# Optimization experiments

Hardware: AMD Instinct MI355X
Metric: run time of the kernel (lower is better)

## Reference

```python
import math
import jax, jax.numpy as jnp
import numpy as np

B, NH, L0 = 16, 128, 16384
KS, STRIDE = 4, 2
INIT_GATE_BIAS = 1.0


def _num_steps(L, ks, stride):
    # number of reduce steps until any N <= L reaches N <= 1 (matches torch N recurrence)
    d, n = 0, L
    while True:
        n = (max(n - ks, 0) + stride - 1) // stride + 1
        d += 1
        if n <= 1:
            return d


def setup_inputs() -> dict:
    key = jax.random.key(0)
    k1, k2, k3, k4 = jax.random.split(key, 4)
    h = jax.random.normal(k1, (B, NH, L0), dtype=jnp.float32)
    N = jax.random.randint(k2, (B,), 1, L0 + 1, dtype=jnp.int32)
    cin = NH + 1  # depth_variant adds one channel
    bound = 1.0 / math.sqrt(cin * KS)
    W = jax.random.uniform(k3, (3 * NH, cin, KS), minval=-bound, maxval=bound, dtype=jnp.float32)
    b = jax.random.uniform(k4, (3 * NH,), minval=-bound, maxval=bound, dtype=jnp.float32)
    b = b.at[2 * NH:].set(INIT_GATE_BIAS)
    return {"h": h, "N": N, "W": W, "b": b}


def _step(h, N, depth, W, b):
    Bb, _, Lc = h.shape
    # depth channel (depth_variant=True), then mask invalid positions (mask applied after concat, as in torch)
    d = jnp.full((Bb, 1, Lc), math.log1p(depth), dtype=h.dtype)
    hh = jnp.concatenate([h, d], axis=1)
    mask = (jnp.arange(Lc) < N[:, None]).astype(hh.dtype)  # [B, Lc]
    hh = hh * mask[:, None, :]
    # right-pad so conv covers all valid positions
    if Lc < KS:
        pad_r = KS - Lc
    elif (Lc - KS) % STRIDE != 0:
        pad_r = STRIDE - (Lc - KS) % STRIDE
    else:
        pad_r = 0
    if pad_r:
        hh = jnp.pad(hh, ((0, 0), (0, 0), (0, pad_r)))
    lrg = jax.lax.conv_general_dilated(
        hh, W, window_strides=(STRIDE,), padding='VALID',
        dimension_numbers=('NCH', 'OIH', 'NCH')) + b[None, :, None]
    l = lrg[:, :NH]
    r = jnp.tanh(lrg[:, NH:2 * NH])
    g = jax.nn.sigmoid(lrg[:, 2 * NH:])
    h_new = l * g + r * (1.0 - g)
    m = jnp.maximum(N - KS, 0)
    N_new = (m + STRIDE - 1) // STRIDE + 1  # ceil(clamp(N-ks,0)/stride)+1
    return h_new, N_new


def reference(h, N, W, b):
    # Fixed-depth unroll: instead of compacting the batch (dynamic shapes), run
    # every sample for all D steps and record its row at the step it finishes.
    # Torch output order = samples sorted stably by finish depth (boolean-index
    # compaction preserves original relative order), reproduced via stable argsort.
    D = _num_steps(h.shape[2], KS, STRIDE)
    Bb = h.shape[0]
    out_h = jnp.zeros((Bb, NH), dtype=h.dtype)
    finish = jnp.full((Bb,), D, dtype=jnp.int32)
    done = jnp.zeros((Bb,), dtype=bool)
    for depth in range(D):
        h, N = _step(h, N, depth, W, b)
        newly = (~done) & (N <= 1)
        out_h = jnp.where(newly[:, None], h[:, :, 0], out_h)
        finish = jnp.where(newly, depth, finish)
        done = done | newly
    order = jnp.argsort(finish)  # stable by default in jax
    return out_h[order]
```

## Files before the change

kernel.cpp:

```cpp
#include <hip/hip_runtime.h>
#include <math.h>

typedef _Float16 f16_t;
typedef _Float16 f16x8 __attribute__((ext_vector_type(8)));
typedef _Float16 f16x4 __attribute__((ext_vector_type(4)));
typedef float    f32x4 __attribute__((ext_vector_type(4)));

#define NHC 128
#define NBATCH 16
#define JT 64
#define THREADS 512
#define TTHREADS 256
#define L0LEN 16384
#define LDSROWPITCH 272
#define LDSREGION (66*LDSROWPITCH)
#define TREG (130*LDSROWPITCH)

__device__ __host__ __forceinline__ int nstep_f(int n){ int m = n - 4; m = m < 0 ? 0 : m; return ((m + 1) >> 1) + 1; }

__global__ void prep_kernel(const float* __restrict__ W, const float* __restrict__ bin,
                            f16_t* __restrict__ Wt, float* __restrict__ Pp, float* __restrict__ biasf)
{
    int c = blockIdx.x;
    int i = threadIdx.x;
    #pragma unroll
    for (int k = 0; k < 4; k++)
        Wt[((size_t)k*384 + c)*128 + i] = (f16_t)W[((size_t)c*129 + i)*4 + k];
    if (i == 0) {
        float s = 0.f;
        Pp[c*5 + 0] = 0.f;
        #pragma unroll
        for (int k = 0; k < 4; k++) { s += W[((size_t)c*129 + 128)*4 + k]; Pp[c*5 + k + 1] = s; }
        biasf[c] = bin[c];
    }
}

template<int CTM>
__device__ __forceinline__ void gemm_tap(f32x4 (&acc)[3][4], const f16_t* __restrict__ Wt,
                                         const char* ldsIn, int arow, int n16, int q)
{
    #pragma unroll 1
    for (int k = 0; k < 4; k++) {
        const f16_t* ab = Wt + ((size_t)k*384 + arow)*128 + q*8;
        f16x8 a0[4], a1[4], a2[4];
        #pragma unroll
        for (int kc = 0; kc < 4; kc++) {
            a0[kc] = *(const f16x8*)(ab + kc*32);
            a1[kc] = *(const f16x8*)(ab + 16384 + kc*32);
            a2[kc] = *(const f16x8*)(ab + 32768 + kc*32);
        }
        const char* bb0 = ldsIn + (k&1)*LDSREGION + ((k>>1) + n16)*LDSROWPITCH + q*16;
        #pragma unroll
        for (int kc = 0; kc < 4; kc++) {
            #pragma unroll
            for (int ct = 0; ct < CTM; ct++) {
                f16x8 bb = *(const f16x8*)(bb0 + ct*(16*LDSROWPITCH) + kc*64);
                acc[0][ct] = __builtin_amdgcn_mfma_f32_16x16x32_f16(a0[kc], bb, acc[0][ct], 0, 0, 0);
                acc[1][ct] = __builtin_amdgcn_mfma_f32_16x16x32_f16(a1[kc], bb, acc[1][ct], 0, 0, 0);
                acc[2][ct] = __builtin_amdgcn_mfma_f32_16x16x32_f16(a2[kc], bb, acc[2][ct], 0, 0, 0);
            }
        }
    }
}

__device__ __forceinline__ void load_biasp(float (&biasr)[3][4], float (&pfull)[3][4],
                                           const float* __restrict__ biasf,
                                           const float* __restrict__ Pp, int cw)
{
    #pragma unroll
    for (int s = 0; s < 3; s++)
        #pragma unroll
        for (int r = 0; r < 4; r++) {
            int row = s*128 + cw + r;
            biasr[s][r] = biasf[row];
            pfull[s][r] = Pp[row*5 + 4];
        }
}

__global__ __launch_bounds__(THREADS) void conv_kernel(
    const float* __restrict__ h, const f16_t* __restrict__ Xin, f16_t* __restrict__ Xout,
    const f16_t* __restrict__ Wt, const float* __restrict__ Pp,
    const float* __restrict__ biasf, const int* __restrict__ N0,
    float* __restrict__ outbuf,
    int t, int inCols, int outCols, float dval)
{
    __shared__ alignas(16) char ldsX[2*LDSREGION];
    const int b  = blockIdx.y;
    const int j0 = blockIdx.x * JT;
    const int tid = threadIdx.x;
    int Nt = N0[b];
    for (int s = 0; s < t; s++) Nt = nstep_f(Nt);
    const int Nt1 = nstep_f(Nt);

    f16_t* XoutB = Xout + ((size_t)b*outCols + j0)*NHC;
    if (j0 >= Nt1) {
        if (j0 <= Nt1 + 1 && tid < 32) {
            float4 z = {0.f,0.f,0.f,0.f};
            ((float4*)XoutB)[tid] = z;
        }
        return;
    }

    if (t == 0) {
        const float* hB = h + (size_t)b*NHC*L0LEN;
        const int P0 = 2*j0;
        const int jpr = tid & 63;
        const int s8  = tid >> 6;
        #pragma unroll
        for (int cg = 0; cg < 16; cg++) {
            int c = cg*8 + s8;
            int p = P0 + jpr*2;
            float2 v = {0.f, 0.f};
            if (p + 1 < Nt)      v = *(const float2*)(hB + (size_t)c*L0LEN + p);
            else if (p < Nt)     v.x = hB[(size_t)c*L0LEN + p];
            char* wb = ldsX + jpr*LDSROWPITCH + c*2;
            *(f16_t*)(wb)             = (f16_t)v.x;
            *(f16_t*)(wb + LDSREGION) = (f16_t)v.y;
        }
        if (tid < 128) {
            int c = tid;
            int p = P0 + 128;
            float2 v = {0.f, 0.f};
            if (p + 1 < Nt)      v = *(const float2*)(hB + (size_t)c*L0LEN + p);
            else if (p < Nt)     v.x = hB[(size_t)c*L0LEN + p];
            char* wb = ldsX + 64*LDSROWPITCH + c*2;
            *(f16_t*)(wb)             = (f16_t)v.x;
            *(f16_t*)(wb + LDSREGION) = (f16_t)v.y;
        }
    } else {
        const char* XinB = (const char*)(Xin + ((size_t)b*inCols + 2*(size_t)j0)*NHC);
        const int maxrow = inCols - 2*j0;
        for (int it = 0; it < 5; ++it) {
            int idx = it*THREADS + tid;
            if (idx < 130*16) {
                int row = idx >> 4, cb = (idx & 15) * 16;
                float4 v = {0.f,0.f,0.f,0.f};
                if (row < maxrow) v = *(const float4*)(XinB + row*256 + cb);
                *(float4*)(ldsX + (row&1)*LDSREGION + (row>>1)*LDSROWPITCH + cb) = v;
            }
        }
    }
    __syncthreads();

    const int w    = tid >> 6;
    const int lane = tid & 63;
    const int n16  = lane & 15;
    const int q    = lane >> 4;
    const int arow = w*16 + n16;
    const int cw   = w*16 + q*4;

    f32x4 acc[3][4] = {};
    int ctm = (Nt1 - j0 + 15) >> 4; if (ctm > 4) ctm = 4;
    switch (ctm) {
    case 1:  gemm_tap<1>(acc, Wt, ldsX, arow, n16, q); break;
    case 2:  gemm_tap<2>(acc, Wt, ldsX, arow, n16, q); break;
    case 3:  gemm_tap<3>(acc, Wt, ldsX, arow, n16, q); break;
    default: gemm_tap<4>(acc, Wt, ldsX, arow, n16, q); break;
    }

    float biasr[3][4], pfull[3][4];
    load_biasp(biasr, pfull, biasf, Pp, cw);

    bool newly = (Nt1 == 1) && (t == 0 || Nt > 1);
    bool record = newly && (j0 == 0);
    float* outrow = outbuf + b*NHC;

    #pragma unroll
    for (int ct = 0; ct < 4; ct++) {
        int j = j0 + ct*16 + n16;
        int cnt = Nt - 2*j; cnt = cnt < 0 ? 0 : (cnt > 4 ? 4 : cnt);
        bool zero = (j >= Nt1);
        float hv[4];
        #pragma unroll
        for (int r = 0; r < 4; r++) {
            float d0, d1, d2;
            if (cnt == 4)      { d0 = pfull[0][r]; d1 = pfull[1][r]; d2 = pfull[2][r]; }
            else if (cnt == 0) { d0 = 0.f; d1 = 0.f; d2 = 0.f; }
            else { int rw = cw + r; d0 = Pp[rw*5 + cnt]; d1 = Pp[(128+rw)*5 + cnt]; d2 = Pp[(256+rw)*5 + cnt]; }
            float lv = acc[0][ct][r] + biasr[0][r] + dval*d0;
            float rp = acc[1][ct][r] + biasr[1][r] + dval*d1;
            float gp = acc[2][ct][r] + biasr[2][r] + dval*d2;
            float e2 = __expf(2.f*rp);
            float rv = 1.f - 2.f/(e2 + 1.f);
            float gv = 1.f/(1.f + __expf(-gp));
            float hh = lv*gv + rv*(1.f - gv);
            hv[r] = zero ? 0.f : hh;
        }
        f16x4 hb;
        #pragma unroll
        for (int r = 0; r < 4; r++) hb[r] = (f16_t)hv[r];
        *(f16x4*)(XoutB + (ct*16 + n16)*NHC + cw) = hb;
        if (record && ct == 0 && n16 == 0) {
            #pragma unroll
            for (int r = 0; r < 4; r++) outrow[cw + r] = hv[r];
        }
    }
}

__global__ __launch_bounds__(TTHREADS, 1) void tail_kernel(
    const f16_t* __restrict__ Xin, const f16_t* __restrict__ Wt,
    const float* __restrict__ Pp, const float* __restrict__ biasf,
    const int* __restrict__ N0, float* __restrict__ outbuf, int inCols)
{
    __shared__ alignas(16) char ldsX[2*TREG + (384 + 1920)*4];
    float* ldsBias = (float*)(ldsX + 2*TREG);
    float* ldsPp   = ldsBias + 384;
    const int b = blockIdx.x;
    const int tid = threadIdx.x;
    int Nt = N0[b];
    #pragma unroll
    for (int s = 0; s < 6; s++) Nt = nstep_f(Nt);
    if (Nt <= 1) return;

    const int w    = tid >> 6;
    const int lane = tid & 63;
    const int n16  = lane & 15;
    const int q    = lane >> 4;
    const int arow = w*16 + n16;
    const int cw   = w*16 + q*4;
    float* outrow  = outbuf + b*NHC;

    f16x8 A[2][4][4][3];
    #pragma unroll
    for (int rg = 0; rg < 2; rg++) {
        #pragma unroll
        for (int k = 0; k < 4; k++) {
            const f16_t* ab = Wt + ((size_t)k*384 + arow + rg*64)*128 + q*8;
            #pragma unroll
            for (int kc = 0; kc < 4; kc++) {
                A[rg][k][kc][0] = *(const f16x8*)(ab + kc*32);
                A[rg][k][kc][1] = *(const f16x8*)(ab + 16384 + kc*32);
                A[rg][k][kc][2] = *(const f16x8*)(ab + 32768 + kc*32);
            }
        }
    }

    const char* XinB = (const char*)(Xin + (size_t)b*inCols*NHC);
    for (int it = 0; it < 17; ++it) {
        int idx = it*TTHREADS + tid;
        if (idx < 258*16) {
            int row = idx >> 4, cb = (idx & 15) * 16;
            float4 v = {0.f,0.f,0.f,0.f};
            if (row < inCols) v = *(const float4*)(XinB + row*256 + cb);
            *(float4*)(ldsX + (row&1)*TREG + (row>>1)*LDSROWPITCH + cb) = v;
        }
    }
    for (int i = tid; i < 384;  i += TTHREADS) ldsBias[i] = biasf[i];
    for (int i = tid; i < 1920; i += TTHREADS) ldsPp[i]   = Pp[i];
    __syncthreads();

    for (int t = 6; t < 13; ++t) {
        int Nt1 = nstep_f(Nt);
        bool newly = (Nt1 == 1);
        float dval = log1pf((float)t);
        int np = (Nt1 >> 4) + 1; if (np > 8) np = 8;
        for (int p = 0; p < np; ++p) {
            f32x4 acc[2][3] = {};
            #pragma unroll
            for (int k = 0; k < 4; k++) {
                const char* bb0 = ldsX + (k&1)*TREG + ((k>>1) + p*16 + n16)*LDSROWPITCH + q*16;
                #pragma unroll
                for (int kc = 0; kc < 4; kc++) {
                    f16x8 bb = *(const f16x8*)(bb0 + kc*64);
                    #pragma unroll
                    for (int rg = 0; rg < 2; rg++) {
                        acc[rg][0] = __builtin_amdgcn_mfma_f32_16x16x32_f16(A[rg][k][kc][0], bb, acc[rg][0], 0, 0, 0);
                        acc[rg][1] = __builtin_amdgcn_mfma_f32_16x16x32_f16(A[rg][k][kc][1], bb, acc[rg][1], 0, 0, 0);
                        acc[rg][2] = __builtin_amdgcn_mfma_f32_16x16x32_f16(A[rg][k][kc][2], bb, acc[rg][2], 0, 0, 0);
                    }
                }
            }
            __syncthreads();

            int j = p*16 + n16;
            int cnt = Nt - 2*j; cnt = cnt < 0 ? 0 : (cnt > 4 ? 4 : cnt);
            bool zero = (j >= Nt1);
            #pragma unroll
            for (int rg = 0; rg < 2; rg++) {
                int cwr = cw + rg*64;
                float hv[4];
                #pragma unroll
                for (int r = 0; r < 4; r++) {
                    int row = cwr + r;
                    float lv = acc[rg][0][r] + ldsBias[row]       + dval*ldsPp[row*5 + cnt];
                    float rp = acc[rg][1][r] + ldsBias[128 + row] + dval*ldsPp[(128 + row)*5 + cnt];
                    float gp = acc[rg][2][r] + ldsBias[256 + row] + dval*ldsPp[(256 + row)*5 + cnt];
                    float e2 = __expf(2.f*rp);
                    float rv = 1.f - 2.f/(e2 + 1.f);
                    float gv = 1.f/(1.f + __expf(-gp));
                    float hh = lv*gv + rv*(1.f - gv);
                    hv[r] = zero ? 0.f : hh;
                }
                f16x4 hb;
                #pragma unroll
                for (int r = 0; r < 4; r++) hb[r] = (f16_t)hv[r];
                *(f16x4*)(ldsX + (j&1)*TREG + (j>>1)*LDSROWPITCH + cwr*2) = hb;
                if (newly && p == 0 && n16 == 0) {
                    #pragma unroll
                    for (int r = 0; r < 4; r++) outrow[cwr + r] = hv[r];
                }
            }
        }
        if (newly) return;
        Nt = Nt1;
        __syncthreads();
    }
}

__global__ void finalize_kernel(const float* __restrict__ outbuf,
                                const int* __restrict__ N0, float* __restrict__ dout)
{
    __shared__ int fin[16];
    __shared__ int rnk[16];
    int tid = threadIdx.x;
    if (tid < 16) {
        int n = N0[tid]; int f = 12;
        for (int t = 0; t < 13; t++) { n = nstep_f(n); if (n == 1) { f = t; break; } }
        fin[tid] = f;
    }
    __syncthreads();
    if (tid < 16) {
        int r = 0;
        for (int b2 = 0; b2 < 16; b2++)
            if (fin[b2] < fin[tid] || (fin[b2] == fin[tid] && b2 < tid)) r++;
        rnk[tid] = r;
    }
    __syncthreads();
    for (int e = tid; e < NBATCH*NHC; e += 256) {
        int b = e >> 7, c = e & 127;
        dout[rnk[b]*NHC + c] = outbuf[e];
    }
}

extern "C" void kernel_launch(void* const* d_in, const int* in_sizes, int n_in,
                              void* d_out, int out_size, void* d_ws, size_t ws_size,
                              hipStream_t stream)
{
    const float* h    = (const float*)d_in[0];
    const int*   N0   = (const int*)d_in[1];
    const float* W    = (const float*)d_in[2];
    const float* bvec = (const float*)d_in[3];
    float* dout = (float*)d_out;

    int Ls[14], Ms[14];
    Ls[0] = L0LEN;
    for (int t = 0; t < 13; t++) Ls[t+1] = nstep_f(Ls[t]);
    for (int t = 0; t < 14; t++) Ms[t] = ((Ls[t] + 63) / 64) * 64;

    char* ws = (char*)d_ws;
    size_t off = 0;
    auto alloc = [&](size_t bytes){ size_t o = off; off += (bytes + 255) & ~(size_t)255; return o; };
    size_t oXA   = alloc((size_t)NBATCH * Ms[1] * NHC * 2);
    size_t oXB   = alloc((size_t)NBATCH * Ms[2] * NHC * 2);
    size_t oWt   = alloc((size_t)4*384*128*2);
    size_t oPp   = alloc((size_t)384*5*4);
    size_t oBias = alloc((size_t)384*4);
    size_t oOut  = alloc((size_t)NBATCH*NHC*4);
    f16_t* XA    = (f16_t*)(ws + oXA);
    f16_t* XB    = (f16_t*)(ws + oXB);
    f16_t* Wt    = (f16_t*)(ws + oWt);
    float* Pp    = (float*)(ws + oPp);
    float* biasf = (float*)(ws + oBias);
    float* outb  = (float*)(ws + oOut);

    hipLaunchKernelGGL(prep_kernel, dim3(384), dim3(128), 0, stream, W, bvec, Wt, Pp, biasf);

    f16_t* cur = XA; f16_t* nxt = XB;
    hipLaunchKernelGGL(conv_kernel, dim3(Ms[1]/JT, NBATCH), dim3(THREADS), 0, stream,
                       h, (const f16_t*)nullptr, XA, Wt, Pp, biasf, N0, outb,
                       0, Ms[0], Ms[1], log1pf(0.f));
    for (int t = 1; t < 6; t++) {
        hipLaunchKernelGGL(conv_kernel, dim3(Ms[t+1]/JT, NBATCH), dim3(THREADS), 0, stream,
                           h, cur, nxt, Wt, Pp, biasf, N0, outb, t, Ms[t], Ms[t+1], log1pf((float)t));
        f16_t* tmp = cur; cur = nxt; nxt = tmp;
    }
    hipLaunchKernelGGL(tail_kernel, dim3(NBATCH), dim3(TTHREADS), 0, stream,
                       cur, Wt, Pp, biasf, N0, outb, Ms[6]);
    hipLaunchKernelGGL(finalize_kernel, dim3(1), dim3(256), 0, stream, outb, N0, dout);
}
```

Before: 438.6 us.

## Make conv kernel persistent with register-resident weights and LDS bias tables

Replaces the one-block-per-tile conv launch with a persistent grid of a few blocks per batch that loop over column tiles. Each 256-thread block keeps a 128-row slice of the f16 weights in registers for all four taps, loaded once, instead of reloading weights from global memory per tile. Bias and partial-sum tables are staged in LDS, and the t==0 load packs eight channels per LDS store. The trade-off is very high register pressure at one block per CU and far fewer blocks in flight, which can leave the GPU underfilled and stop load latency being hidden.

```diff
diff --git a/kernel.cpp b/kernel.cpp
--- a/kernel.cpp
+++ b/kernel.cpp
@@ -9,7 +9,7 @@
 #define NHC 128
 #define NBATCH 16
 #define JT 64
-#define THREADS 512
+#define CTHREADS 256
 #define TTHREADS 256
 #define L0LEN 16384
 #define LDSROWPITCH 272
@@ -35,112 +35,31 @@
     }
 }
 
-template<int CTM>
-__device__ __forceinline__ void gemm_tap(f32x4 (&acc)[3][4], const f16_t* __restrict__ Wt,
-                                         const char* ldsIn, int arow, int n16, int q)
-{
-    #pragma unroll 1
-    for (int k = 0; k < 4; k++) {
-        const f16_t* ab = Wt + ((size_t)k*384 + arow)*128 + q*8;
-        f16x8 a0[4], a1[4], a2[4];
-        #pragma unroll
-        for (int kc = 0; kc < 4; kc++) {
-            a0[kc] = *(const f16x8*)(ab + kc*32);
-            a1[kc] = *(const f16x8*)(ab + 16384 + kc*32);
-            a2[kc] = *(const f16x8*)(ab + 32768 + kc*32);
-        }
-        const char* bb0 = ldsIn + (k&1)*LDSREGION + ((k>>1) + n16)*LDSROWPITCH + q*16;
-        #pragma unroll
-        for (int kc = 0; kc < 4; kc++) {
-            #pragma unroll
-            for (int ct = 0; ct < CTM; ct++) {
-                f16x8 bb = *(const f16x8*)(bb0 + ct*(16*LDSROWPITCH) + kc*64);
-                acc[0][ct] = __builtin_amdgcn_mfma_f32_16x16x32_f16(a0[kc], bb, acc[0][ct], 0, 0, 0);
-                acc[1][ct] = __builtin_amdgcn_mfma_f32_16x16x32_f16(a1[kc], bb, acc[1][ct], 0, 0, 0);
-                acc[2][ct] = __builtin_amdgcn_mfma_f32_16x16x32_f16(a2[kc], bb, acc[2][ct], 0, 0, 0);
-            }
-        }
-    }
-}
-
-__device__ __forceinline__ void load_biasp(float (&biasr)[3][4], float (&pfull)[3][4],
-                                           const float* __restrict__ biasf,
-                                           const float* __restrict__ Pp, int cw)
-{
-    #pragma unroll
-    for (int s = 0; s < 3; s++)
-        #pragma unroll
-        for (int r = 0; r < 4; r++) {
-            int row = s*128 + cw + r;
-            biasr[s][r] = biasf[row];
-            pfull[s][r] = Pp[row*5 + 4];
-        }
-}
-
-__global__ __launch_bounds__(THREADS) void conv_kernel(
+__global__ __launch_bounds__(CTHREADS, 1) void conv_kernel(
     const float* __restrict__ h, const f16_t* __restrict__ Xin, f16_t* __restrict__ Xout,
     const f16_t* __restrict__ Wt, const float* __restrict__ Pp,
     const float* __restrict__ biasf, const int* __restrict__ N0,
     float* __restrict__ outbuf,
     int t, int inCols, int outCols, float dval)
 {
-    __shared__ alignas(16) char ldsX[2*LDSREGION];
+    __shared__ alignas(16) char ldsX[2*LDSREGION + (384 + 1920)*4];
+    float* ldsBias = (float*)(ldsX + 2*LDSREGION);
+    float* ldsPp   = ldsBias + 384;
     const int b  = blockIdx.y;
-    const int j0 = blockIdx.x * JT;
+    const int bx = blockIdx.x;
+    const int G  = gridDim.x;
     const int tid = threadIdx.x;
     int Nt = N0[b];
     for (int s = 0; s < t; s++) Nt = nstep_f(Nt);
     const int Nt1 = nstep_f(Nt);
 
-    f16_t* XoutB = Xout + ((size_t)b*outCols + j0)*NHC;
-    if (j0 >= Nt1) {
-        if (j0 <= Nt1 + 1 && tid < 32) {
+    if (bx*JT >= Nt1) {
+        if (bx*JT <= Nt1 + 1 && tid < 32) {
             float4 z = {0.f,0.f,0.f,0.f};
-            ((float4*)XoutB)[tid] = z;
+            ((float4*)(Xout + ((size_t)b*outCols + (size_t)bx*JT)*NHC))[tid] = z;
         }
         return;
     }
-
-    if (t == 0) {
-        const float* hB = h + (size_t)b*NHC*L0LEN;
-        const int P0 = 2*j0;
-        const int jpr = tid & 63;
-        const int s8  = tid >> 6;
-        #pragma unroll
-        for (int cg = 0; cg < 16; cg++) {
-            int c = cg*8 + s8;
-            int p = P0 + jpr*2;
-            float2 v = {0.f, 0.f};
-            if (p + 1 < Nt)      v = *(const float2*)(hB + (size_t)c*L0LEN + p);
-            else if (p < Nt)     v.x = hB[(size_t)c*L0LEN + p];
-            char* wb = ldsX + jpr*LDSROWPITCH + c*2;
-            *(f16_t*)(wb)             = (f16_t)v.x;
-            *(f16_t*)(wb + LDSREGION) = (f16_t)v.y;
-        }
-        if (tid < 128) {
-            int c = tid;
-            int p = P0 + 128;
-            float2 v = {0.f, 0.f};
-            if (p + 1 < Nt)      v = *(const float2*)(hB + (size_t)c*L0LEN + p);
-            else if (p < Nt)     v.x = hB[(size_t)c*L0LEN + p];
-            char* wb = ldsX + 64*LDSROWPITCH + c*2;
-            *(f16_t*)(wb)             = (f16_t)v.x;
-            *(f16_t*)(wb + LDSREGION) = (f16_t)v.y;
-        }
-    } else {
-        const char* XinB = (const char*)(Xin + ((size_t)b*inCols + 2*(size_t)j0)*NHC);
-        const int maxrow = inCols - 2*j0;
-        for (int it = 0; it < 5; ++it) {
-            int idx = it*THREADS + tid;
-            if (idx < 130*16) {
-                int row = idx >> 4, cb = (idx & 15) * 16;
-                float4 v = {0.f,0.f,0.f,0.f};
-                if (row < maxrow) v = *(const float4*)(XinB + row*256 + cb);
-                *(float4*)(ldsX + (row&1)*LDSREGION + (row>>1)*LDSROWPITCH + cb) = v;
-            }
-        }
-    }
-    __syncthreads();
 
     const int w    = tid >> 6;
     const int lane = tid & 63;
@@ -148,52 +67,137 @@
     const int q    = lane >> 4;
     const int arow = w*16 + n16;
     const int cw   = w*16 + q*4;
-
-    f32x4 acc[3][4] = {};
-    int ctm = (Nt1 - j0 + 15) >> 4; if (ctm > 4) ctm = 4;
-    switch (ctm) {
-    case 1:  gemm_tap<1>(acc, Wt, ldsX, arow, n16, q); break;
-    case 2:  gemm_tap<2>(acc, Wt, ldsX, arow, n16, q); break;
-    case 3:  gemm_tap<3>(acc, Wt, ldsX, arow, n16, q); break;
-    default: gemm_tap<4>(acc, Wt, ldsX, arow, n16, q); break;
-    }
-
-    float biasr[3][4], pfull[3][4];
-    load_biasp(biasr, pfull, biasf, Pp, cw);
-
-    bool newly = (Nt1 == 1) && (t == 0 || Nt > 1);
-    bool record = newly && (j0 == 0);
-    float* outrow = outbuf + b*NHC;
-
+    float* outrow  = outbuf + b*NHC;
+    const bool newly = (Nt1 == 1) && (t == 0 || Nt > 1);
+
+    f16x8 A[2][4][4][3];
     #pragma unroll
-    for (int ct = 0; ct < 4; ct++) {
-        int j = j0 + ct*16 + n16;
-        int cnt = Nt - 2*j; cnt = cnt < 0 ? 0 : (cnt > 4 ? 4 : cnt);
-        bool zero = (j >= Nt1);
-        float hv[4];
+    for (int rg = 0; rg < 2; rg++) {
         #pragma unroll
-        for (int r = 0; r < 4; r++) {
-            float d0, d1, d2;
-            if (cnt == 4)      { d0 = pfull[0][r]; d1 = pfull[1][r]; d2 = pfull[2][r]; }
-            else if (cnt == 0) { d0 = 0.f; d1 = 0.f; d2 = 0.f; }
-            else { int rw = cw + r; d0 = Pp[rw*5 + cnt]; d1 = Pp[(128+rw)*5 + cnt]; d2 = Pp[(256+rw)*5 + cnt]; }
-            float lv = acc[0][ct][r] + biasr[0][r] + dval*d0;
-            float rp = acc[1][ct][r] + biasr[1][r] + dval*d1;
-            float gp = acc[2][ct][r] + biasr[2][r] + dval*d2;
-            float e2 = __expf(2.f*rp);
-            float rv = 1.f - 2.f/(e2 + 1.f);
-            float gv = 1.f/(1.f + __expf(-gp));
-            float hh = lv*gv + rv*(1.f - gv);
-            hv[r] = zero ? 0.f : hh;
-        }
-        f16x4 hb;
-        #pragma unroll
-        for (int r = 0; r < 4; r++) hb[r] = (f16_t)hv[r];
-        *(f16x4*)(XoutB + (ct*16 + n16)*NHC + cw) = hb;
-        if (record && ct == 0 && n16 == 0) {
-            #pragma unroll
-            for (int r = 0; r < 4; r++) outrow[cw + r] = hv[r];
-        }
+        for (int k = 0; k < 4; k++) {
+            const f16_t* ab = Wt + ((size_t)k*384 + arow + rg*64)*128 + q*8;
+            #pragma unroll
+            for (int kc = 0; kc < 4; kc++) {
+                A[rg][k][kc][0] = *(const f16x8*)(ab + kc*32);
+                A[rg][k][kc][1] = *(const f16x8*)(ab + 16384 + kc*32);
+                A[rg][k][kc][2] = *(const f16x8*)(ab + 32768 + kc*32);
+            }
+        }
+    }
+    for (int i = tid; i < 384;  i += CTHREADS) ldsBias[i] = biasf[i];
+    for (int i = tid; i < 1920; i += CTHREADS) ldsPp[i]   = Pp[i];
+
+    for (int jt = bx; ; jt += G) {
+        const int j0 = jt*JT;
+        if (j0 >= outCols) break;
+        f16_t* XoutB = Xout + ((size_t)b*outCols + j0)*NHC;
+        if (j0 >= Nt1) {
+            if (j0 <= Nt1 + 1 && tid < 32) {
+                float4 z = {0.f,0.f,0.f,0.f};
+                ((float4*)XoutB)[tid] = z;
+            }
+            break;
+        }
+
+        if (t == 0) {
+            const float* hB = h + (size_t)b*NHC*L0LEN;
+            const int P0 = 2*j0;
+            const int pr  = tid & 63;
+            const int ws4 = tid >> 6;
+            const int p   = P0 + pr*2;
+            const bool full = (p + 1 < Nt), half = (p < Nt);
+            #pragma unroll 1
+            for (int g = 0; g < 4; g++) {
+                const int cbase = ws4*32 + g*8;
+                f16x8 ev, od;
+                #pragma unroll
+                for (int e = 0; e < 8; e++) {
+                    float2 v = {0.f, 0.f};
+                    if (full)      v = *(const float2*)(hB + (size_t)(cbase + e)*L0LEN + p);
+                    else if (half) v.x = hB[(size_t)(cbase + e)*L0LEN + p];
+                    ev[e] = (f16_t)v.x; od[e] = (f16_t)v.y;
+                }
+                char* wb = ldsX + pr*LDSROWPITCH + cbase*2;
+                *(f16x8*)(wb)             = ev;
+                *(f16x8*)(wb + LDSREGION) = od;
+            }
+            if (tid < 16) {
+                const int cb8 = tid*8;
+                const int ph  = P0 + 128;
+                f16x8 ev, od;
+                #pragma unroll
+                for (int e = 0; e < 8; e++) {
+                    float2 v = {0.f, 0.f};
+                    if (ph + 1 < Nt)      v = *(const float2*)(hB + (size_t)(cb8 + e)*L0LEN + ph);
+                    else if (ph < Nt)     v.x = hB[(size_t)(cb8 + e)*L0LEN + ph];
+                    ev[e] = (f16_t)v.x; od[e] = (f16_t)v.y;
+                }
+                char* wb = ldsX + 64*LDSROWPITCH + cb8*2;
+                *(f16x8*)(wb)             = ev;
+                *(f16x8*)(wb + LDSREGION) = od;
+            }
+        } else {
+            const char* XinB = (const char*)(Xin + ((size_t)b*inCols + 2*(size_t)j0)*NHC);
+            const int maxrow = inCols - 2*j0;
+            for (int it = 0; it < 9; ++it) {
+                int idx = it*CTHREADS + tid;
+                if (idx < 130*16) {
+                    int row = idx >> 4, cb = (idx & 15) * 16;
+                    float4 v = {0.f,0.f,0.f,0.f};
+                    if (row < maxrow) v = *(const float4*)(XinB + row*256 + cb);
+                    *(float4*)(ldsX + (row&1)*LDSREGION + (row>>1)*LDSROWPITCH + cb) = v;
+                }
+            }
+        }
+        __syncthreads();
+
+        int npass = (Nt1 - j0 + 15) >> 4; if (npass > 4) npass = 4;
+        for (int p = 0; p < npass; ++p) {
+            f32x4 acc[2][3] = {};
+            #pragma unroll
+            for (int k = 0; k < 4; k++) {
+                const char* bb0 = ldsX + (k&1)*LDSREGION + ((k>>1) + p*16 + n16)*LDSROWPITCH + q*16;
+                #pragma unroll
+                for (int kc = 0; kc < 4; kc++) {
+                    f16x8 bb = *(const f16x8*)(bb0 + kc*64);
+                    #pragma unroll
+                    for (int rg = 0; rg < 2; rg++) {
+                        acc[rg][0] = __builtin_amdgcn_mfma_f32_16x16x32_f16(A[rg][k][kc][0], bb, acc[rg][0], 0, 0, 0);
+                        acc[rg][1] = __builtin_amdgcn_mfma_f32_16x16x32_f16(A[rg][k][kc][1], bb, acc[rg][1], 0, 0, 0);
+                        acc[rg][2] = __builtin_amdgcn_mfma_f32_16x16x32_f16(A[rg][k][kc][2], bb, acc[rg][2], 0, 0, 0);
+                    }
+                }
+            }
+            int j = j0 + p*16 + n16;
+            int cnt = Nt - 2*j; cnt = cnt < 0 ? 0 : (cnt > 4 ? 4 : cnt);
+            bool zero = (j >= Nt1);
+            #pragma unroll
+            for (int rg = 0; rg < 2; rg++) {
+                int cwr = cw + rg*64;
+                float hv[4];
+                #pragma unroll
+                for (int r = 0; r < 4; r++) {
+                    int row = cwr + r;
+                    float lv = acc[rg][0][r] + ldsBias[row]       + dval*ldsPp[row*5 + cnt];
+                    float rp = acc[rg][1][r] + ldsBias[128 + row] + dval*ldsPp[(128 + row)*5 + cnt];
+                    float gp = acc[rg][2][r] + ldsBias[256 + row] + dval*ldsPp[(256 + row)*5 + cnt];
+                    float e2 = __expf(2.f*rp);
+                    float rv = 1.f - 2.f/(e2 + 1.f);
+                    float gv = 1.f/(1.f + __expf(-gp));
+                    float hh = lv*gv + rv*(1.f - gv);
+                    hv[r] = zero ? 0.f : hh;
+                }
+                f16x4 hb;
+                #pragma unroll
+                for (int r = 0; r < 4; r++) hb[r] = (f16_t)hv[r];
+                *(f16x4*)(XoutB + (p*16 + n16)*NHC + cwr) = hb;
+                if (newly && j0 == 0 && p == 0 && n16 == 0) {
+                    #pragma unroll
+                    for (int r = 0; r < 4; r++) outrow[cwr + r] = hv[r];
+                }
+            }
+        }
+        __syncthreads();
     }
 }
 
@@ -365,12 +369,14 @@
 
     hipLaunchKernelGGL(prep_kernel, dim3(384), dim3(128), 0, stream, W, bvec, Wt, Pp, biasf);
 
+    const int Gt[6] = {16, 16, 16, 16, 8, 4};
+
     f16_t* cur = XA; f16_t* nxt = XB;
-    hipLaunchKernelGGL(conv_kernel, dim3(Ms[1]/JT, NBATCH), dim3(THREADS), 0, stream,
+    hipLaunchKernelGGL(conv_kernel, dim3(Gt[0], NBATCH), dim3(CTHREADS), 0, stream,
                        h, (const f16_t*)nullptr, XA, Wt, Pp, biasf, N0, outb,
                        0, Ms[0], Ms[1], log1pf(0.f));
     for (int t = 1; t < 6; t++) {
-        hipLaunchKernelGGL(conv_kernel, dim3(Ms[t+1]/JT, NBATCH), dim3(THREADS), 0, stream,
+        hipLaunchKernelGGL(conv_kernel, dim3(Gt[t], NBATCH), dim3(CTHREADS), 0, stream,
                            h, cur, nxt, Wt, Pp, biasf, N0, outb, t, Ms[t], Ms[t+1], log1pf((float)t));
         f16_t* tmp = cur; cur = nxt; nxt = tmp;
     }
```

Result: slower. 604.4 us (+37.8%).

## Fuse pairs of strided conv steps into one kernel via LDS intermediate

Applied to the files above, without the earlier changes.

Adds a fused_kernel that computes two consecutive conv/gate reduction steps per block: it loads a wider input window (262 rows), computes the intermediate level into LDS, then produces the second-level output. Steps 0-1 and 2-3 now use it, which removes the global write and read of the step-1 and step-3 activations and two kernel launches. In exchange, each fused block recomputes two overlapping boundary intermediate rows and does extra MFMA work on a padded third group. It also uses more LDS per block, which may reduce occupancy.

```diff
diff --git a/kernel.cpp b/kernel.cpp
--- a/kernel.cpp
+++ b/kernel.cpp
@@ -15,6 +15,8 @@
 #define LDSROWPITCH 272
 #define LDSREGION (66*LDSROWPITCH)
 #define TREG (130*LDSROWPITCH)
+#define RIN  (146*LDSROWPITCH)
+#define RMID (73*LDSROWPITCH)
 
 __device__ __host__ __forceinline__ int nstep_f(int n){ int m = n - 4; m = m < 0 ? 0 : m; return ((m + 1) >> 1) + 1; }
 
@@ -35,9 +37,9 @@
     }
 }
 
-template<int CTM>
+template<int REG, int CTM>
 __device__ __forceinline__ void gemm_tap(f32x4 (&acc)[3][4], const f16_t* __restrict__ Wt,
-                                         const char* ldsIn, int arow, int n16, int q)
+                                         const char* ldsIn, int arow, int n16, int q, int jt)
 {
     #pragma unroll 1
     for (int k = 0; k < 4; k++) {
@@ -49,7 +51,7 @@
             a1[kc] = *(const f16x8*)(ab + 16384 + kc*32);
             a2[kc] = *(const f16x8*)(ab + 32768 + kc*32);
         }
-        const char* bb0 = ldsIn + (k&1)*LDSREGION + ((k>>1) + n16)*LDSROWPITCH + q*16;
+        const char* bb0 = ldsIn + (k&1)*REG + ((k>>1) + n16 + jt*16)*LDSROWPITCH + q*16;
         #pragma unroll
         for (int kc = 0; kc < 4; kc++) {
             #pragma unroll
@@ -75,6 +77,160 @@
             biasr[s][r] = biasf[row];
             pfull[s][r] = Pp[row*5 + 4];
         }
+}
+
+__device__ __forceinline__ float gate_f(float lv, float rp, float gp)
+{
+    float e2 = __expf(2.f*rp);
+    float rv = 1.f - 2.f/(e2 + 1.f);
+    float gv = 1.f/(1.f + __expf(-gp));
+    return lv*gv + rv*(1.f - gv);
+}
+
+__global__ __launch_bounds__(THREADS) void fused_kernel(
+    const float* __restrict__ h, const f16_t* __restrict__ Xin, f16_t* __restrict__ Xout,
+    const f16_t* __restrict__ Wt, const float* __restrict__ Pp,
+    const float* __restrict__ biasf, const int* __restrict__ N0,
+    float* __restrict__ outbuf,
+    int t, int inCols, int outCols, float dval1, float dval2)
+{
+    __shared__ alignas(16) char lds[2*RIN + 2*RMID];
+    char* mid = lds + 2*RIN;
+    const int b  = blockIdx.y;
+    const int j0 = blockIdx.x * JT;
+    const int tid = threadIdx.x;
+    int Nt = N0[b];
+    for (int s = 0; s < t; s++) Nt = nstep_f(Nt);
+    const int Nt1 = nstep_f(Nt);
+    const int Nt2 = nstep_f(Nt1);
+
+    f16_t* XoutB = Xout + ((size_t)b*outCols + j0)*NHC;
+    if (j0 >= Nt2) {
+        if (j0 <= Nt2 + 1 && tid < 32) {
+            float4 z = {0.f,0.f,0.f,0.f};
+            ((float4*)XoutB)[tid] = z;
+        }
+        return;
+    }
+
+    if (t == 0) {
+        const float* hB = h + (size_t)b*NHC*L0LEN;
+        const int P0 = 4*j0;
+        const int jpr0 = tid & 63;
+        const int s8   = tid >> 6;
+        for (int it = 0; it < 3; ++it) {
+            int pr = jpr0 + it*64;
+            if (pr < 146) {
+                int p = P0 + pr*2;
+                bool full = (p + 1 < Nt), half = (p < Nt);
+                #pragma unroll
+                for (int cg = 0; cg < 16; cg++) {
+                    int c = cg*8 + s8;
+                    float2 v = {0.f, 0.f};
+                    if (full)      v = *(const float2*)(hB + (size_t)c*L0LEN + p);
+                    else if (half) v.x = hB[(size_t)c*L0LEN + p];
+                    char* wb = lds + pr*LDSROWPITCH + c*2;
+                    *(f16_t*)(wb)       = (f16_t)v.x;
+                    *(f16_t*)(wb + RIN) = (f16_t)v.y;
+                }
+            }
+        }
+    } else {
+        const char* XinB = (const char*)(Xin + ((size_t)b*inCols + 4*(size_t)j0)*NHC);
+        const int maxrow = inCols - 4*j0;
+        for (int it = 0; it < 9; ++it) {
+            int idx = it*THREADS + tid;
+            if (idx < 262*16) {
+                int row = idx >> 4, cb = (idx & 15) * 16;
+                float4 v = {0.f,0.f,0.f,0.f};
+                if (row < maxrow) v = *(const float4*)(XinB + row*256 + cb);
+                *(float4*)(lds + (row&1)*RIN + (row>>1)*LDSROWPITCH + cb) = v;
+            }
+        }
+    }
+    __syncthreads();
+
+    const int w    = tid >> 6;
+    const int lane = tid & 63;
+    const int n16  = lane & 15;
+    const int q    = lane >> 4;
+    const int arow = w*16 + n16;
+    const int cw   = w*16 + q*4;
+    float* outrow  = outbuf + b*NHC;
+
+    float biasr[3][4], pfull[3][4];
+    load_biasp(biasr, pfull, biasf, Pp, cw);
+
+    const bool newly1 = (Nt1 == 1) && (t == 0 || Nt > 1);
+    const bool newly2 = (Nt2 == 1) && (Nt1 > 1);
+
+    #pragma unroll 1
+    for (int g = 0; g < 3; ++g) {
+        const int ctmg = (g < 2) ? 4 : 1;
+        f32x4 acc[3][4] = {};
+        switch (ctmg) {
+        case 4: gemm_tap<RIN,4>(acc, Wt, lds, arow, n16, q, g*4); break;
+        default: gemm_tap<RIN,1>(acc, Wt, lds, arow, n16, q, g*4); break;
+        }
+        for (int ct = 0; ct < ctmg; ++ct) {
+            int j1loc = g*64 + ct*16 + n16;
+            int j1 = 2*j0 + j1loc;
+            int cnt = Nt - 2*j1; cnt = cnt < 0 ? 0 : (cnt > 4 ? 4 : cnt);
+            bool zero = (j1 >= Nt1) || (j1loc >= 130);
+            float hv[4];
+            #pragma unroll
+            for (int r = 0; r < 4; r++) {
+                float d0, d1, d2;
+                if (cnt == 4)      { d0 = pfull[0][r]; d1 = pfull[1][r]; d2 = pfull[2][r]; }
+                else if (cnt == 0) { d0 = 0.f; d1 = 0.f; d2 = 0.f; }
+                else { int rw = cw + r; d0 = Pp[rw*5 + cnt]; d1 = Pp[(128+rw)*5 + cnt]; d2 = Pp[(256+rw)*5 + cnt]; }
+                float hh = gate_f(acc[0][ct][r] + biasr[0][r] + dval1*d0,
+                                  acc[1][ct][r] + biasr[1][r] + dval1*d1,
+                                  acc[2][ct][r] + biasr[2][r] + dval1*d2);
+                hv[r] = zero ? 0.f : hh;
+            }
+            f16x4 hb;
+            #pragma unroll
+            for (int r = 0; r < 4; r++) hb[r] = (f16_t)hv[r];
+            *(f16x4*)(mid + (j1loc&1)*RMID + (j1loc>>1)*LDSROWPITCH + cw*2) = hb;
+            if (newly1 && j0 == 0 && g == 0 && ct == 0 && n16 == 0) {
+                #pragma unroll
+                for (int r = 0; r < 4; r++) outrow[cw + r] = hv[r];
+            }
+        }
+    }
+    __syncthreads();
+
+    {
+        f32x4 acc[3][4] = {};
+        gemm_tap<RMID,4>(acc, Wt, mid, arow, n16, q, 0);
+        #pragma unroll
+        for (int ct = 0; ct < 4; ++ct) {
+            int j = j0 + ct*16 + n16;
+            int cnt = Nt1 - 2*j; cnt = cnt < 0 ? 0 : (cnt > 4 ? 4 : cnt);
+            bool zero = (j >= Nt2);
+            float hv[4];
+            #pragma unroll
+            for (int r = 0; r < 4; r++) {
+                float d0, d1, d2;
+                if (cnt == 4)      { d0 = pfull[0][r]; d1 = pfull[1][r]; d2 = pfull[2][r]; }
+                else if (cnt == 0) { d0 = 0.f; d1 = 0.f; d2 = 0.f; }
+                else { int rw = cw + r; d0 = Pp[rw*5 + cnt]; d1 = Pp[(128+rw)*5 + cnt]; d2 = Pp[(256+rw)*5 + cnt]; }
+                float hh = gate_f(acc[0][ct][r] + biasr[0][r] + dval2*d0,
+                                  acc[1][ct][r] + biasr[1][r] + dval2*d1,
+                                  acc[2][ct][r] + biasr[2][r] + dval2*d2);
+                hv[r] = zero ? 0.f : hh;
+            }
+            f16x4 hb;
+            #pragma unroll
+            for (int r = 0; r < 4; r++) hb[r] = (f16_t)hv[r];
+            *(f16x4*)(XoutB + (ct*16 + n16)*NHC + cw) = hb;
+            if (newly2 && j0 == 0 && ct == 0 && n16 == 0) {
+                #pragma unroll
+                for (int r = 0; r < 4; r++) outrow[cw + r] = hv[r];
+            }
+        }
+    }
 }
 
 __global__ __launch_bounds__(THREADS) void conv_kernel(
@@ -101,33 +257,7 @@
         return;
     }
 
-    if (t == 0) {
-        const float* hB = h + (size_t)b*NHC*L0LEN;
-        const int P0 = 2*j0;
-        const int jpr = tid & 63;
-        const int s8  = tid >> 6;
-        #pragma unroll
-        for (int cg = 0; cg < 16; cg++) {
-            int c = cg*8 + s8;
-            int p = P0 + jpr*2;
-            float2 v = {0.f, 0.f};
-            if (p + 1 < Nt)      v = *(const float2*)(hB + (size_t)c*L0LEN + p);
-            else if (p < Nt)     v.x = hB[(size_t)c*L0LEN + p];
-            char* wb = ldsX + jpr*LDSROWPITCH + c*2;
-            *(f16_t*)(wb)             = (f16_t)v.x;
-            *(f16_t*)(wb + LDSREGION) = (f16_t)v.y;
-        }
-        if (tid < 128) {
-            int c = tid;
-            int p = P0 + 128;
-            float2 v = {0.f, 0.f};
-            if (p + 1 < Nt)      v = *(const float2*)(hB + (size_t)c*L0LEN + p);
-            else if (p < Nt)     v.x = hB[(size_t)c*L0LEN + p];
-            char* wb = ldsX + 64*LDSROWPITCH + c*2;
-            *(f16_t*)(wb)             = (f16_t)v.x;
-            *(f16_t*)(wb + LDSREGION) = (f16_t)v.y;
-        }
-    } else {
+    {
         const char* XinB = (const char*)(Xin + ((size_t)b*inCols + 2*(size_t)j0)*NHC);
         const int maxrow = inCols - 2*j0;
         for (int it = 0; it < 5; ++it) {
@@ -152,16 +282,16 @@
     f32x4 acc[3][4] = {};
     int ctm = (Nt1 - j0 + 15) >> 4; if (ctm > 4) ctm = 4;
     switch (ctm) {
-    case 1:  gemm_tap<1>(acc, Wt, ldsX, arow, n16, q); break;
-    case 2:  gemm_tap<2>(acc, Wt, ldsX, arow, n16, q); break;
-    case 3:  gemm_tap<3>(acc, Wt, ldsX, arow, n16, q); break;
-    default: gemm_tap<4>(acc, Wt, ldsX, arow, n16, q); break;
+    case 1:  gemm_tap<LDSREGION,1>(acc, Wt, ldsX, arow, n16, q, 0); break;
+    case 2:  gemm_tap<LDSREGION,2>(acc, Wt, ldsX, arow, n16, q, 0); break;
+    case 3:  gemm_tap<LDSREGION,3>(acc, Wt, ldsX, arow, n16, q, 0); break;
+    default: gemm_tap<LDSREGION,4>(acc, Wt, ldsX, arow, n16, q, 0); break;
     }
 
     float biasr[3][4], pfull[3][4];
     load_biasp(biasr, pfull, biasf, Pp, cw);
 
-    bool newly = (Nt1 == 1) && (t == 0 || Nt > 1);
+    bool newly = (Nt1 == 1) && (Nt > 1);
     bool record = newly && (j0 == 0);
     float* outrow = outbuf + b*NHC;
 
@@ -177,13 +307,9 @@
             if (cnt == 4)      { d0 = pfull[0][r]; d1 = pfull[1][r]; d2 = pfull[2][r]; }
             else if (cnt == 0) { d0 = 0.f; d1 = 0.f; d2 = 0.f; }
             else { int rw = cw + r; d0 = Pp[rw*5 + cnt]; d1 = Pp[(128+rw)*5 + cnt]; d2 = Pp[(256+rw)*5 + cnt]; }
-            float lv = acc[0][ct][r] + biasr[0][r] + dval*d0;
-            float rp = acc[1][ct][r] + biasr[1][r] + dval*d1;
-            float gp = acc[2][ct][r] + biasr[2][r] + dval*d2;
-            float e2 = __expf(2.f*rp);
-            float rv = 1.f - 2.f/(e2 + 1.f);
-            float gv = 1.f/(1.f + __expf(-gp));
-            float hh = lv*gv + rv*(1.f - gv);
+            float hh = gate_f(acc[0][ct][r] + biasr[0][r] + dval*d0,
+                              acc[1][ct][r] + biasr[1][r] + dval*d1,
+                              acc[2][ct][r] + biasr[2][r] + dval*d2);
             hv[r] = zero ? 0.f : hh;
         }
         f16x4 hb;
@@ -282,13 +408,9 @@
                 #pragma unroll
                 for (int r = 0; r < 4; r++) {
                     int row = cwr + r;
-                    float lv = acc[rg][0][r] + ldsBias[row]       + dval*ldsPp[row*5 + cnt];
-                    float rp = acc[rg][1][r] + ldsBias[128 + row] + dval*ldsPp[(128 + row)*5 + cnt];
-                    float gp = acc[rg][2][r] + ldsBias[256 + row] + dval*ldsPp[(256 + row)*5 + cnt];
-                    float e2 = __expf(2.f*rp);
-                    float rv = 1.f - 2.f/(e2 + 1.f);
-                    float gv = 1.f/(1.f + __expf(-gp));
-                    float hh = lv*gv + rv*(1.f - gv);
+                    float hh = gate_f(acc[rg][0][r] + ldsBias[row]       + dval*ldsPp[row*5 + cnt],
+                                      acc[rg][1][r] + ldsBias[128 + row] + dval*ldsPp[(128 + row)*5 + cnt],
+                                      acc[rg][2][r] + ldsBias[256 + row] + dval*ldsPp[(256 + row)*5 + cnt]);
                     hv[r] = zero ? 0.f : hh;
                 }
                 f16x4 hb;
@@ -350,14 +472,18 @@
     char* ws = (char*)d_ws;
     size_t off = 0;
     auto alloc = [&](size_t bytes){ size_t o = off; off += (bytes + 255) & ~(size_t)255; return o; };
-    size_t oXA   = alloc((size_t)NBATCH * Ms[1] * NHC * 2);
-    size_t oXB   = alloc((size_t)NBATCH * Ms[2] * NHC * 2);
+    size_t oX2 = alloc((size_t)NBATCH * Ms[2] * NHC * 2);
+    size_t oX4 = alloc((size_t)NBATCH * Ms[4] * NHC * 2);
+    size_t oX5 = alloc((size_t)NBATCH * Ms[5] * NHC * 2);
+    size_t oX6 = alloc((size_t)NBATCH * Ms[6] * NHC * 2);
     size_t oWt   = alloc((size_t)4*384*128*2);
     size_t oPp   = alloc((size_t)384*5*4);
     size_t oBias = alloc((size_t)384*4);
     size_t oOut  = alloc((size_t)NBATCH*NHC*4);
-    f16_t* XA    = (f16_t*)(ws + oXA);
-    f16_t* XB    = (f16_t*)(ws + oXB);
+    f16_t* X2 = (f16_t*)(ws + oX2);
+    f16_t* X4 = (f16_t*)(ws + oX4);
+    f16_t* X5 = (f16_t*)(ws + oX5);
+    f16_t* X6 = (f16_t*)(ws + oX6);
     f16_t* Wt    = (f16_t*)(ws + oWt);
     float* Pp    = (float*)(ws + oPp);
     float* biasf = (float*)(ws + oBias);
@@ -365,16 +491,17 @@
 
     hipLaunchKernelGGL(prep_kernel, dim3(384), dim3(128), 0, stream, W, bvec, Wt, Pp, biasf);
 
-    f16_t* cur = XA; f16_t* nxt = XB;
-    hipLaunchKernelGGL(conv_kernel, dim3(Ms[1]/JT, NBATCH), dim3(THREADS), 0, stream,
-                       h, (const f16_t*)nullptr, XA, Wt, Pp, biasf, N0, outb,
-                       0, Ms[0], Ms[1], log1pf(0.f));
-    for (int t = 1; t < 6; t++) {
-        hipLaunchKernelGGL(conv_kernel, dim3(Ms[t+1]/JT, NBATCH), dim3(THREADS), 0, stream,
-                           h, cur, nxt, Wt, Pp, biasf, N0, outb, t, Ms[t], Ms[t+1], log1pf((float)t));
-        f16_t* tmp = cur; cur = nxt; nxt = tmp;
-    }
+    hipLaunchKernelGGL(fused_kernel, dim3(Ms[2]/JT, NBATCH), dim3(THREADS), 0, stream,
+                       h, (const f16_t*)nullptr, X2, Wt, Pp, biasf, N0, outb,
+                       0, Ms[0], Ms[2], log1pf(0.f), log1pf(1.f));
+    hipLaunchKernelGGL(fused_kernel, dim3(Ms[4]/JT, NBATCH), dim3(THREADS), 0, stream,
+                       h, X2, X4, Wt, Pp, biasf, N0, outb,
+                       2, Ms[2], Ms[4], log1pf(2.f), log1pf(3.f));
+    hipLaunchKernelGGL(conv_kernel, dim3(Ms[5]/JT, NBATCH), dim3(THREADS), 0, stream,
+                       h, X4, X5, Wt, Pp, biasf, N0, outb, 4, Ms[4], Ms[5], log1pf(4.f));
+    hipLaunchKernelGGL(conv_kernel, dim3(Ms[6]/JT, NBATCH), dim3(THREADS), 0, stream,
+                       h, X5, X6, Wt, Pp, biasf, N0, outb, 5, Ms[5], Ms[6], log1pf(5.f));
     hipLaunchKernelGGL(tail_kernel, dim3(NBATCH), dim3(TTHREADS), 0, stream,
-                       cur, Wt, Pp, biasf, N0, outb, Ms[6]);
+                       X6, Wt, Pp, biasf, N0, outb, Ms[6]);
     hipLaunchKernelGGL(finalize_kernel, dim3(1), dim3(256), 0, stream, outb, N0, dout);
 }
```

After: 583.1 us. 32.9% more time.
